# Kernel optimization log

Measured on AMD Instinct MI355X. Metric: run time of the kernel, lower is better.

## Reference

```python
import jax, jax.numpy as jnp
import numpy as np

GAMMA = 0.1
N_CENTERS = 1024
INPUT_DIM = 64
BATCH = 65536


def setup_inputs() -> dict:
    key = jax.random.key(0)
    kx, kc = jax.random.split(key)
    x = jax.random.normal(kx, (BATCH, INPUT_DIM), dtype=jnp.float32)
    # centers ~ Uniform(0, 1), matching torch.empty(...).uniform_(0, 1)
    centers = jax.random.uniform(kc, (N_CENTERS, INPUT_DIM), dtype=jnp.float32)
    return {"x": x, "centers": centers}


def reference(x, centers):
    # Pairwise squared L2 distance via the matmul expansion trick:
    x_sq = jnp.sum(x * x, axis=-1, keepdims=True)          # [B, 1]
    c_sq = jnp.sum(centers * centers, axis=-1)             # [N]
    cross = jnp.einsum("bd,nd->bn", x, centers)            # [B, N]
    l2 = x_sq + c_sq[None, :] - 2.0 * cross                # [B, N]
    l2 = jnp.maximum(l2, 0.0)  # guard tiny negatives from the expansion
    return jnp.exp(-GAMMA * l2)
```

## Files before the change

### kernel.cpp

```cpp
#include <hip/hip_runtime.h>

#define GAMMA 0.1f

constexpr int MTOT = 65536;
constexpr int NTOT = 1024;
constexpr int KDIM = 64;
constexpr int RPB  = 256;
constexpr int SUB  = 32;
constexpr int NSUB = RPB / SUB;

using f16x8 = __attribute__((ext_vector_type(8))) _Float16;
using f16x4 = __attribute__((ext_vector_type(4))) _Float16;
using f32x4 = __attribute__((ext_vector_type(4))) float;

__global__ __launch_bounds__(1024, 4)
void rbf_fused_kernel(const float* __restrict__ x,
                      const float* __restrict__ centers,
                      float* __restrict__ out) {
  __shared__ _Float16 sCen[NTOT * KDIM];
  __shared__ _Float16 sX[2][SUB * KDIM];
  __shared__ float    sCsq[NTOT];
  __shared__ float    sXsq[2][SUB];

  const int tid = threadIdx.x;
  const int mb = blockIdx.x;

  const float4* xsrc = reinterpret_cast<const float4*>(x + (size_t)mb * RPB * KDIM);

  auto convert_x = [&](float4 v4, int buf) {
    const int row = tid >> 4;
    const int f15 = tid & 15;
    const int s = f15 >> 1;
    const int half = f15 & 1;
    const float vv[4] = {v4.x, v4.y, v4.z, v4.w};
    f16x4 hv;
    float ss = 0.0f;
    #pragma unroll
    for (int e = 0; e < 4; ++e) {
      hv[e] = (_Float16)vv[e];
      ss += vv[e] * vv[e];
    }
    ss += __shfl_xor(ss, 1);
    ss += __shfl_xor(ss, 2);
    ss += __shfl_xor(ss, 4);
    ss += __shfl_xor(ss, 8);
    if (f15 == 0) sXsq[buf][row] = ss;
    const int slot = s ^ (row & 7);
    *reinterpret_cast<f16x4*>(&sX[buf][row * KDIM + slot * 8 + half * 4]) = hv;
  };

  float4 rx;
  if (tid < 512) rx = xsrc[tid];

  {
    const float4* cf = reinterpret_cast<const float4*>(centers);
    #pragma unroll
    for (int p = 0; p < 8; ++p) {
      const int c = p * 1024 + tid;
      const int row = c >> 3;
      const int s = c & 7;
      const float4 v0 = cf[c * 2];
      const float4 v1 = cf[c * 2 + 1];
      const float v[8] = {v0.x, v0.y, v0.z, v0.w, v1.x, v1.y, v1.z, v1.w};
      f16x8 hv;
      float ss = 0.0f;
      #pragma unroll
      for (int i = 0; i < 8; ++i) {
        hv[i] = (_Float16)v[i];
        ss += v[i] * v[i];
      }
      ss += __shfl_xor(ss, 1);
      ss += __shfl_xor(ss, 2);
      ss += __shfl_xor(ss, 4);
      if (s == 0) sCsq[row] = ss;
      const int slot = s ^ (row & 7);
      *reinterpret_cast<f16x8*>(&sCen[row * KDIM + slot * 8]) = hv;
    }
  }
  if (tid < 512) {
    convert_x(rx, 0);
    rx = xsrc[512 + tid];
  }
  __syncthreads();

  const int lane = tid & 63;
  const int wave = tid >> 6;
  const int wm = wave & 1;
  const int wn = wave >> 1;
  const int l = lane & 15;
  const int g = lane >> 4;

  #pragma unroll 1
  for (int jt = 0; jt < NSUB; ++jt) {
    const int b = jt & 1;

    if (jt + 1 < NSUB && tid < 512) convert_x(rx, b ^ 1);
    if (jt + 2 < NSUB && tid < 512) rx = xsrc[(jt + 2) * 512 + tid];

    const int xrow = wm * 16 + l;
    f16x8 xh[2];
    #pragma unroll
    for (int ks = 0; ks < 2; ++ks) {
      const int slot = (ks * 4 + g) ^ (l & 7);
      xh[ks] = *reinterpret_cast<const f16x8*>(&sX[b][xrow * KDIM + slot * 8]);
    }
    const float xs = sXsq[b][xrow];

    const size_t rowg = (size_t)mb * RPB + jt * SUB + wm * 16 + l;
    float* orow = out + rowg * (size_t)NTOT + wn * 128;

    #pragma unroll
    for (int nf = 0; nf < 8; ++nf) {
      const int crow = wn * 128 + nf * 16 + l;
      f32x4 acc = {};
      #pragma unroll
      for (int ks = 0; ks < 2; ++ks) {
        const int slot = (ks * 4 + g) ^ (l & 7);
        const f16x8 ch = *reinterpret_cast<const f16x8*>(&sCen[crow * KDIM + slot * 8]);
        acc = __builtin_amdgcn_mfma_f32_16x16x32_f16(ch, xh[ks], acc, 0, 0, 0);
      }
      const float4 cs = *reinterpret_cast<const float4*>(&sCsq[wn * 128 + nf * 16 + g * 4]);
      float4 o;
      o.x = __expf(-GAMMA * fmaxf(xs + cs.x - 2.0f * acc[0], 0.0f));
      o.y = __expf(-GAMMA * fmaxf(xs + cs.y - 2.0f * acc[1], 0.0f));
      o.z = __expf(-GAMMA * fmaxf(xs + cs.z - 2.0f * acc[2], 0.0f));
      o.w = __expf(-GAMMA * fmaxf(xs + cs.w - 2.0f * acc[3], 0.0f));
      *reinterpret_cast<float4*>(orow + nf * 16 + g * 4) = o;
    }

    if (jt + 1 < NSUB) {
      asm volatile("s_waitcnt lgkmcnt(0)" ::: "memory");
      __builtin_amdgcn_s_barrier();
      __builtin_amdgcn_sched_barrier(0);
    }
  }
}

extern "C" void kernel_launch(void* const* d_in, const int* in_sizes, int n_in,
                              void* d_out, int out_size, void* d_ws, size_t ws_size,
                              hipStream_t stream) {
  (void)in_sizes; (void)n_in; (void)d_ws; (void)ws_size; (void)out_size;
  const float* x       = (const float*)d_in[0];
  const float* centers = (const float*)d_in[1];
  float* out = (float*)d_out;
  rbf_fused_kernel<<<MTOT / RPB, 1024, 0, stream>>>(x, centers, out);
}
```

Baseline: 59.39 us.

## Give each wave 16 x rows held in registers and sweep all centers

Each of the 16 waves now owns 16 x rows and loads them straight from global memory into registers as fp16 fragments. It computes the row norms with lane shuffles, then sweeps all 1024 centers held in LDS. This drops the double-buffered x staging in shared memory and the per-subtile barriers. The trade is that all x loads are issued up front and each wave writes whole output rows over a long loop, which can change how well the stores coalesce and overlap.

```diff
diff --git a/kernel.cpp b/kernel.cpp
--- a/kernel.cpp
+++ b/kernel.cpp
@@ -6,51 +6,31 @@
 constexpr int NTOT = 1024;
 constexpr int KDIM = 64;
 constexpr int RPB  = 256;
-constexpr int SUB  = 32;
-constexpr int NSUB = RPB / SUB;
 
 using f16x8 = __attribute__((ext_vector_type(8))) _Float16;
-using f16x4 = __attribute__((ext_vector_type(4))) _Float16;
 using f32x4 = __attribute__((ext_vector_type(4))) float;
 
 __global__ __launch_bounds__(1024, 4)
-void rbf_fused_kernel(const float* __restrict__ x,
+void rbf_sweep_kernel(const float* __restrict__ x,
                       const float* __restrict__ centers,
                       float* __restrict__ out) {
   __shared__ _Float16 sCen[NTOT * KDIM];
-  __shared__ _Float16 sX[2][SUB * KDIM];
   __shared__ float    sCsq[NTOT];
-  __shared__ float    sXsq[2][SUB];
 
   const int tid = threadIdx.x;
   const int mb = blockIdx.x;
+  const int lane = tid & 63;
+  const int wave = tid >> 6;
+  const int l = lane & 15;
+  const int g = lane >> 4;
 
-  const float4* xsrc = reinterpret_cast<const float4*>(x + (size_t)mb * RPB * KDIM);
-
-  auto convert_x = [&](float4 v4, int buf) {
-    const int row = tid >> 4;
-    const int f15 = tid & 15;
-    const int s = f15 >> 1;
-    const int half = f15 & 1;
-    const float vv[4] = {v4.x, v4.y, v4.z, v4.w};
-    f16x4 hv;
-    float ss = 0.0f;
-    #pragma unroll
-    for (int e = 0; e < 4; ++e) {
-      hv[e] = (_Float16)vv[e];
-      ss += vv[e] * vv[e];
-    }
-    ss += __shfl_xor(ss, 1);
-    ss += __shfl_xor(ss, 2);
-    ss += __shfl_xor(ss, 4);
-    ss += __shfl_xor(ss, 8);
-    if (f15 == 0) sXsq[buf][row] = ss;
-    const int slot = s ^ (row & 7);
-    *reinterpret_cast<f16x4*>(&sX[buf][row * KDIM + slot * 8 + half * 4]) = hv;
-  };
-
-  float4 rx;
-  if (tid < 512) rx = xsrc[tid];
+  const float* xrp = x + ((size_t)mb * RPB + wave * 16 + l) * KDIM;
+  float4 xr[4];
+  #pragma unroll
+  for (int ks = 0; ks < 2; ++ks) {
+    xr[ks * 2]     = *reinterpret_cast<const float4*>(xrp + ks * 32 + g * 8);
+    xr[ks * 2 + 1] = *reinterpret_cast<const float4*>(xrp + ks * 32 + g * 8 + 4);
+  }
 
   {
     const float4* cf = reinterpret_cast<const float4*>(centers);
@@ -77,62 +57,43 @@
       *reinterpret_cast<f16x8*>(&sCen[row * KDIM + slot * 8]) = hv;
     }
   }
-  if (tid < 512) {
-    convert_x(rx, 0);
-    rx = xsrc[512 + tid];
-  }
   __syncthreads();
 
-  const int lane = tid & 63;
-  const int wave = tid >> 6;
-  const int wm = wave & 1;
-  const int wn = wave >> 1;
-  const int l = lane & 15;
-  const int g = lane >> 4;
+  f16x8 xh[2];
+  float ss = 0.0f;
+  #pragma unroll
+  for (int ks = 0; ks < 2; ++ks) {
+    const float v[8] = {xr[ks*2].x,   xr[ks*2].y,   xr[ks*2].z,   xr[ks*2].w,
+                        xr[ks*2+1].x, xr[ks*2+1].y, xr[ks*2+1].z, xr[ks*2+1].w};
+    f16x8 h;
+    #pragma unroll
+    for (int e = 0; e < 8; ++e) {
+      h[e] = (_Float16)v[e];
+      ss += v[e] * v[e];
+    }
+    xh[ks] = h;
+  }
+  ss += __shfl_xor(ss, 16);
+  ss += __shfl_xor(ss, 32);
 
-  #pragma unroll 1
-  for (int jt = 0; jt < NSUB; ++jt) {
-    const int b = jt & 1;
-
-    if (jt + 1 < NSUB && tid < 512) convert_x(rx, b ^ 1);
-    if (jt + 2 < NSUB && tid < 512) rx = xsrc[(jt + 2) * 512 + tid];
-
-    const int xrow = wm * 16 + l;
-    f16x8 xh[2];
+  float* orow = out + ((size_t)mb * RPB + wave * 16 + l) * (size_t)NTOT;
+  #pragma unroll 8
+  for (int nf = 0; nf < 64; ++nf) {
+    const int crow = nf * 16 + l;
+    f32x4 acc = {};
     #pragma unroll
     for (int ks = 0; ks < 2; ++ks) {
       const int slot = (ks * 4 + g) ^ (l & 7);
-      xh[ks] = *reinterpret_cast<const f16x8*>(&sX[b][xrow * KDIM + slot * 8]);
+      const f16x8 ch = *reinterpret_cast<const f16x8*>(&sCen[crow * KDIM + slot * 8]);
+      acc = __builtin_amdgcn_mfma_f32_16x16x32_f16(ch, xh[ks], acc, 0, 0, 0);
     }
-    const float xs = sXsq[b][xrow];
-
-    const size_t rowg = (size_t)mb * RPB + jt * SUB + wm * 16 + l;
-    float* orow = out + rowg * (size_t)NTOT + wn * 128;
-
-    #pragma unroll
-    for (int nf = 0; nf < 8; ++nf) {
-      const int crow = wn * 128 + nf * 16 + l;
-      f32x4 acc = {};
-      #pragma unroll
-      for (int ks = 0; ks < 2; ++ks) {
-        const int slot = (ks * 4 + g) ^ (l & 7);
-        const f16x8 ch = *reinterpret_cast<const f16x8*>(&sCen[crow * KDIM + slot * 8]);
-        acc = __builtin_amdgcn_mfma_f32_16x16x32_f16(ch, xh[ks], acc, 0, 0, 0);
-      }
-      const float4 cs = *reinterpret_cast<const float4*>(&sCsq[wn * 128 + nf * 16 + g * 4]);
-      float4 o;
-      o.x = __expf(-GAMMA * fmaxf(xs + cs.x - 2.0f * acc[0], 0.0f));
-      o.y = __expf(-GAMMA * fmaxf(xs + cs.y - 2.0f * acc[1], 0.0f));
-      o.z = __expf(-GAMMA * fmaxf(xs + cs.z - 2.0f * acc[2], 0.0f));
-      o.w = __expf(-GAMMA * fmaxf(xs + cs.w - 2.0f * acc[3], 0.0f));
-      *reinterpret_cast<float4*>(orow + nf * 16 + g * 4) = o;
-    }
-
-    if (jt + 1 < NSUB) {
-      asm volatile("s_waitcnt lgkmcnt(0)" ::: "memory");
-      __builtin_amdgcn_s_barrier();
-      __builtin_amdgcn_sched_barrier(0);
-    }
+    const float4 cs = *reinterpret_cast<const float4*>(&sCsq[nf * 16 + g * 4]);
+    float4 o;
+    o.x = __expf(-GAMMA * fmaxf(ss + cs.x - 2.0f * acc[0], 0.0f));
+    o.y = __expf(-GAMMA * fmaxf(ss + cs.y - 2.0f * acc[1], 0.0f));
+    o.z = __expf(-GAMMA * fmaxf(ss + cs.z - 2.0f * acc[2], 0.0f));
+    o.w = __expf(-GAMMA * fmaxf(ss + cs.w - 2.0f * acc[3], 0.0f));
+    *reinterpret_cast<float4*>(orow + nf * 16 + g * 4) = o;
   }
 }
 
@@ -143,5 +104,5 @@
   const float* x       = (const float*)d_in[0];
   const float* centers = (const float*)d_in[1];
   float* out = (float*)d_out;
-  rbf_fused_kernel<<<MTOT / RPB, 1024, 0, stream>>>(x, centers, out);
+  rbf_sweep_kernel<<<MTOT / RPB, 1024, 0, stream>>>(x, centers, out);
 }
```

Measured after the change: 55.75 us. 1.07x faster.
